# Performance work log

Hardware: AMD Instinct MI355X
Metric: run time of the kernel (lower is better)

The kernel has to match this reference:

```python
import jax, jax.numpy as jnp
import numpy as np

B, L, H = 4, 512, 768          # batch, seq_len, bert hidden
S, R = 100, 100                # num candidate spans, num relation pairs
E = 128                        # size embedding dim
TE, TR = 8, 6                  # entity / relation types
MAX_ENT_LEN = 100
NEG = -1e20


def _span_masks(rng, b, n, seq_len, max_len):
    # contiguous span masks with lengths in [1, max_len-1] so sum(-1) < max_len
    starts = rng.integers(0, seq_len - 1, size=(b, n))
    lengths = rng.integers(1, max_len, size=(b, n))
    ends = np.minimum(starts + lengths, seq_len)
    pos = np.arange(seq_len)
    m = (pos[None, None, :] >= starts[..., None]) & (pos[None, None, :] < ends[..., None])
    return jnp.asarray(m.astype(np.int32))


def setup_inputs() -> dict:
    rng = np.random.default_rng(0)
    key = jax.random.key(0)
    k = jax.random.split(key, 6)
    return {
        "last_hidden_state": jax.random.normal(k[0], (B, L, H), jnp.float32),
        "entity_mask": _span_masks(rng, B, S, L, MAX_ENT_LEN),
        "relations": jnp.asarray(rng.integers(0, S, size=(B, R, 2)).astype(np.int32)),
        "relation_context_mask": _span_masks(rng, B, R, L, MAX_ENT_LEN),
        "relation_sample_mask": jnp.asarray(rng.integers(0, 2, size=(B, R)).astype(np.int32)),
        "size_emb": jax.random.normal(k[1], (MAX_ENT_LEN, E), jnp.float32) * 0.02,
        "span_w": jax.random.normal(k[2], (E + 2 * H, TE), jnp.float32) * 0.02,
        "span_b": jnp.zeros((TE,), jnp.float32),
        "rel_w": jax.random.normal(k[3], (2 * E + 3 * H, TR), jnp.float32) * 0.02,
        "rel_b": jnp.zeros((TR,), jnp.float32),
    }


def _masked_max(h, mask):
    # h: [B,L,H], mask: [B,N,L] int {0,1} -> [B,N,H]
    mf = mask[..., None].astype(h.dtype)                       # [B,N,L,1]
    masked = jnp.where(mf == 0, jnp.asarray(NEG, h.dtype), h[:, None] * mf)
    return masked.max(axis=2)


def reference(last_hidden_state, entity_mask, relations, relation_context_mask,
              relation_sample_mask, size_emb, span_w, span_b, rel_w, rel_b):
    b = last_hidden_state.shape[0]
    # ---- entity classification ----
    context = last_hidden_state[:, 0]                          # CLS pooling [B,H]
    entity_size = size_emb[entity_mask.sum(-1)]                # [B,S,E]
    entity = _masked_max(last_hidden_state, entity_mask)       # [B,S,H]
    ctx = jnp.broadcast_to(context[:, None], (b, entity.shape[1], context.shape[-1]))
    entity_repr = jnp.concatenate([entity, ctx, entity_size], axis=-1)
    entity_logit = entity_repr @ span_w + span_b               # [B,S,TE]
    # ---- relation classification ----
    rel_ctx = _masked_max(last_hidden_state, relation_context_mask)  # [B,R,H]
    rel_ctx = jnp.where(relation_sample_mask[..., None] == 1,
                        jnp.zeros((), rel_ctx.dtype), rel_ctx)
    r = relations.shape[1]
    flat = relations.reshape(b, r * 2)                         # [B,2R]
    pair = jnp.take_along_axis(entity, flat[..., None], axis=1).reshape(b, r, -1)      # [B,R,2H]
    pair_size = jnp.take_along_axis(entity_size, flat[..., None], axis=1).reshape(b, r, -1)  # [B,R,2E]
    relation_repr = jnp.concatenate([rel_ctx, pair, pair_size], axis=-1)
    relation_logit = relation_repr @ rel_w + rel_b             # [B,R,TR]
    return entity_logit, relation_logit
```

## Files before the change

### kernel.cpp

```cpp
#include <hip/hip_runtime.h>

#define Bn 4
#define Ln 512
#define Hn 768
#define Sn 100
#define Rn 100
#define En 128
#define TEn 8
#define TRn 6
#define NEGF (-1e20f)
#define H4 (Hn / 4)
#define E4 (En / 4)
#define NTHR 640

__device__ __forceinline__ float4 fmax4(float4 a, float4 b) {
    return make_float4(fmaxf(a.x, b.x), fmaxf(a.y, b.y),
                       fmaxf(a.z, b.z), fmaxf(a.w, b.w));
}

__device__ __forceinline__ void scan_span(const int* __restrict__ mask,
                                          int lane, int* start, int* end) {
    const int4* m4 = (const int4*)(mask + lane * 8);
    int4 a = m4[0], c = m4[1];
    int mm[8] = {a.x, a.y, a.z, a.w, c.x, c.y, c.z, c.w};
    int first = 0x7fffffff, last = -1;
    #pragma unroll
    for (int r = 0; r < 8; ++r) {
        if (mm[r] != 0) {
            int row = lane * 8 + r;
            first = min(first, row);
            last = max(last, row);
        }
    }
    #pragma unroll
    for (int off = 1; off < 64; off <<= 1) {
        first = min(first, __shfl_xor(first, off, 64));
        last = max(last, __shfl_xor(last, off, 64));
    }
    *start = first;
    *end = last + 1;
}

__global__ void __launch_bounds__(NTHR)
span_kernel(const float* __restrict__ hid,
            const int* __restrict__ ent_mask,
            const int* __restrict__ rel_mask,
            const int* __restrict__ samp_mask,
            const float* __restrict__ size_emb,
            const float* __restrict__ span_w,
            const float* __restrict__ span_b,
            const float* __restrict__ rel_w,
            float* __restrict__ relpart,
            float* __restrict__ p0ws,
            float* __restrict__ p1ws,
            int* __restrict__ entcnt,
            float* __restrict__ out_ent) {
    int blk = blockIdx.x;
    int tid = threadIdx.x;
    int lane = tid & 63, wv = tid >> 6;
    int grp = tid / 192;
    int u = tid - grp * 192;

    __shared__ float4 sh[3][192];
    __shared__ float red[10][TEn];

    bool is_ent = blk < Bn * Sn;
    int b, rblk = 0;
    const int* mask;
    if (is_ent) {
        b = blk / Sn;
        mask = ent_mask + (size_t)blk * Ln;
    } else {
        rblk = blk - Bn * Sn;
        b = rblk / Rn;
        if (samp_mask[rblk] == 1) {
            if (tid < TRn) relpart[(size_t)rblk * TRn + tid] = 0.f;
            return;
        }
        mask = rel_mask + (size_t)rblk * Ln;
    }

    int start, end;
    scan_span(mask, lane, &start, &end);
    int cnt = end - start;
    if (is_ent && tid == 0) entcnt[blk] = cnt;

    const float4* hb4 = (const float4*)(hid + (size_t)b * Ln * Hn);

    if (grp < 3) {
        const float4* col = hb4 + u;
        float4 m0 = make_float4(NEGF, NEGF, NEGF, NEGF), m1 = m0;
        int r = start + grp;
        for (; r + 3 < end; r += 6) {
            m0 = fmax4(m0, col[(size_t)r * H4]);
            m1 = fmax4(m1, col[(size_t)(r + 3) * H4]);
        }
        if (r < end) m0 = fmax4(m0, col[(size_t)r * H4]);
        sh[grp][u] = fmax4(m0, m1);
    }
    __syncthreads();

    float acc[TEn];
    #pragma unroll
    for (int t = 0; t < TEn; ++t) acc[t] = 0.f;

    bool do_red;
    if (grp < 3) {
        do_red = is_ent || (grp == 0);
        if (do_red) {
            float4 v = fmax4(fmax4(sh[0][u], sh[1][u]), sh[2][u]);
            const float* vp = &v.x;
            if (is_ent) {
                if (grp == 0) {
                    #pragma unroll
                    for (int j = 0; j < 4; ++j) {
                        const float* wr = span_w + (size_t)(4 * u + j) * TEn;
                        #pragma unroll
                        for (int t = 0; t < TEn; ++t) acc[t] += vp[j] * wr[t];
                    }
                } else {
                    int base = (grp == 1 ? Hn : 2 * Hn) + 4 * u;
                    #pragma unroll
                    for (int j = 0; j < 4; ++j) {
                        const float* wr = rel_w + (size_t)(base + j) * TRn;
                        #pragma unroll
                        for (int t = 0; t < TRn; ++t) acc[t] += vp[j] * wr[t];
                    }
                }
            } else {
                #pragma unroll
                for (int j = 0; j < 4; ++j) {
                    const float* wr = rel_w + (size_t)(4 * u + j) * TRn;
                    #pragma unroll
                    for (int t = 0; t < TRn; ++t) acc[t] += vp[j] * wr[t];
                }
            }
        }
    } else {
        do_red = is_ent;
        if (is_ent) {
            #pragma unroll
            for (int cc = 0; cc < 3; ++cc) {
                int c = lane + cc * 64;
                float4 v = hb4[c];
                const float* vp = &v.x;
                #pragma unroll
                for (int j = 0; j < 4; ++j) {
                    const float* wr = span_w + (size_t)(Hn + 4 * c + j) * TEn;
                    #pragma unroll
                    for (int t = 0; t < TEn; ++t) acc[t] += vp[j] * wr[t];
                }
            }
            if (lane < E4) {
                float4 sv = ((const float4*)(size_emb + (size_t)cnt * En))[lane];
                const float* sp = &sv.x;
                #pragma unroll
                for (int j = 0; j < 4; ++j) {
                    const float* wr = span_w + (size_t)(2 * Hn + 4 * lane + j) * TEn;
                    #pragma unroll
                    for (int t = 0; t < TEn; ++t) acc[t] += sp[j] * wr[t];
                }
            }
        }
    }

    if (do_red) {
        #pragma unroll
        for (int t = 0; t < TEn; ++t)
            #pragma unroll
            for (int off = 32; off > 0; off >>= 1)
                acc[t] += __shfl_down(acc[t], off, 64);
        if (lane == 0) {
            #pragma unroll
            for (int t = 0; t < TEn; ++t) red[wv][t] = acc[t];
        }
    }
    __syncthreads();

    if (is_ent) {
        if (tid < TEn) {
            out_ent[(size_t)blk * TEn + tid] = span_b[tid]
                + red[0][tid] + red[1][tid] + red[2][tid] + red[9][tid];
        } else if (tid >= 64 && tid < 64 + TRn) {
            int t = tid - 64;
            p0ws[(size_t)blk * TRn + t] = red[3][t] + red[4][t] + red[5][t];
        } else if (tid >= 128 && tid < 128 + TRn) {
            int t = tid - 128;
            p1ws[(size_t)blk * TRn + t] = red[6][t] + red[7][t] + red[8][t];
        }
    } else {
        if (tid < TRn)
            relpart[(size_t)rblk * TRn + tid] =
                red[0][tid] + red[1][tid] + red[2][tid];
    }
}

__global__ void __launch_bounds__(64)
combine_kernel(const int* __restrict__ relations,
               const int* __restrict__ entcnt,
               const float* __restrict__ size_emb,
               const float* __restrict__ rel_w,
               const float* __restrict__ rel_b,
               const float* __restrict__ relpart,
               const float* __restrict__ p0ws,
               const float* __restrict__ p1ws,
               float* __restrict__ out_rel) {
    int rblk = blockIdx.x;
    int b = rblk / Rn;
    int lane = threadIdx.x;
    int a0 = relations[rblk * 2 + 0];
    int a1 = relations[rblk * 2 + 1];
    int e0 = b * Sn + a0, e1 = b * Sn + a1;

    int c = lane & 31;
    int srow = entcnt[(lane < 32) ? e0 : e1];
    int wbase = (lane < 32) ? 3 * Hn : 3 * Hn + En;

    float acc[TRn];
    #pragma unroll
    for (int t = 0; t < TRn; ++t) acc[t] = 0.f;

    float4 sv = ((const float4*)(size_emb + (size_t)srow * En))[c];
    const float* sp = &sv.x;
    #pragma unroll
    for (int j = 0; j < 4; ++j) {
        const float* wr = rel_w + (size_t)(wbase + 4 * c + j) * TRn;
        #pragma unroll
        for (int t = 0; t < TRn; ++t) acc[t] += sp[j] * wr[t];
    }

    #pragma unroll
    for (int t = 0; t < TRn; ++t)
        #pragma unroll
        for (int off = 32; off > 0; off >>= 1)
            acc[t] += __shfl_down(acc[t], off, 64);

    if (lane == 0) {
        #pragma unroll
        for (int t = 0; t < TRn; ++t) {
            out_rel[(size_t)rblk * TRn + t] = acc[t]
                + relpart[(size_t)rblk * TRn + t]
                + p0ws[(size_t)e0 * TRn + t]
                + p1ws[(size_t)e1 * TRn + t]
                + rel_b[t];
        }
    }
}

extern "C" void kernel_launch(void* const* d_in, const int* in_sizes, int n_in,
                              void* d_out, int out_size, void* d_ws, size_t ws_size,
                              hipStream_t stream) {
    const float* hid       = (const float*)d_in[0];
    const int*   ent_mask  = (const int*)d_in[1];
    const int*   relations = (const int*)d_in[2];
    const int*   rel_mask  = (const int*)d_in[3];
    const int*   samp_mask = (const int*)d_in[4];
    const float* size_emb  = (const float*)d_in[5];
    const float* span_w    = (const float*)d_in[6];
    const float* span_b    = (const float*)d_in[7];
    const float* rel_w     = (const float*)d_in[8];
    const float* rel_b     = (const float*)d_in[9];

    float* out = (float*)d_out;
    float* out_ent = out;
    float* out_rel = out + Bn * Sn * TEn;

    char* ws = (char*)d_ws;
    float* relpart = (float*)ws;
    float* p0ws    = relpart + (size_t)Bn * Rn * TRn;
    float* p1ws    = p0ws + (size_t)Bn * Sn * TRn;
    int*   entcnt  = (int*)(p1ws + (size_t)Bn * Sn * TRn);

    span_kernel<<<Bn * (Sn + Rn), NTHR, 0, stream>>>(
        hid, ent_mask, rel_mask, samp_mask, size_emb, span_w, span_b,
        rel_w, relpart, p0ws, p1ws, entcnt, out_ent);

    combine_kernel<<<Bn * Rn, 64, 0, stream>>>(
        relations, entcnt, size_emb, rel_w, rel_b,
        relpart, p0ws, p1ws, out_rel);
}
```

Baseline: 25.06 us.

## Precompute 8-row block maxima and fold pair-size projections into span kernel

Adds a pre-pass kernel that computes per-8-row block maxima of the hidden states, so each span's masked max reads block maxima for its interior and raw rows only at the ragged edges. The per-entity size-embedding projections onto the relation weights are moved into the span kernel's fourth-group waves. This lets the combine kernel become a simple elementwise gather-add over relations. It trades an extra launch plus a full pass over the hidden tensor for fewer per-span row reads and a lighter final kernel.

```diff
diff --git a/kernel.cpp b/kernel.cpp
--- a/kernel.cpp
+++ b/kernel.cpp
@@ -9,6 +9,8 @@
 #define TEn 8
 #define TRn 6
 #define NEGF (-1e20f)
+#define W 8
+#define NBLK (Ln / W)
 #define H4 (Hn / 4)
 #define E4 (En / 4)
 #define NTHR 640
@@ -16,6 +18,22 @@
 __device__ __forceinline__ float4 fmax4(float4 a, float4 b) {
     return make_float4(fmaxf(a.x, b.x), fmaxf(a.y, b.y),
                        fmaxf(a.z, b.z), fmaxf(a.w, b.w));
+}
+
+__global__ void __launch_bounds__(192)
+blockmax_kernel(const float* __restrict__ hid, float* __restrict__ bmax) {
+    int bj = blockIdx.x;
+    int b = bj / NBLK, j = bj % NBLK;
+    int tid = threadIdx.x;
+    const float4* src = (const float4*)(hid + ((size_t)b * Ln + j * W) * Hn);
+    float4 m0 = src[tid];
+    float4 m1 = src[(size_t)H4 + tid];
+    #pragma unroll
+    for (int r = 2; r < W; r += 2) {
+        m0 = fmax4(m0, src[(size_t)r * H4 + tid]);
+        m1 = fmax4(m1, src[(size_t)(r + 1) * H4 + tid]);
+    }
+    ((float4*)(bmax + (size_t)bj * Hn))[tid] = fmax4(m0, m1);
 }
 
 __device__ __forceinline__ void scan_span(const int* __restrict__ mask,
@@ -39,6 +57,28 @@
     }
     *start = first;
     *end = last + 1;
+}
+
+__device__ __forceinline__ float4 gmax(const float4* __restrict__ hb4,
+                                       const float4* __restrict__ bm4,
+                                       int start, int end, int grp) {
+    float4 m0 = make_float4(NEGF, NEGF, NEGF, NEGF), m1 = m0;
+    int jstart = (start + 7) >> 3, jend = end >> 3;
+    if (jstart >= jend) {
+        for (int r = start + grp; r < end; r += 6) {
+            m0 = fmax4(m0, hb4[(size_t)r * H4]);
+            int r2 = r + 3;
+            if (r2 < end) m1 = fmax4(m1, hb4[(size_t)r2 * H4]);
+        }
+        return fmax4(m0, m1);
+    }
+    for (int j = jstart + grp; j < jend; j += 3)
+        m0 = fmax4(m0, bm4[(size_t)j * H4]);
+    for (int r = start + grp; r < jstart * W; r += 3)
+        m1 = fmax4(m1, hb4[(size_t)r * H4]);
+    for (int r = jend * W + grp; r < end; r += 3)
+        m0 = fmax4(m0, hb4[(size_t)r * H4]);
+    return fmax4(m0, m1);
 }
 
 __global__ void __launch_bounds__(NTHR)
@@ -50,10 +90,10 @@
             const float* __restrict__ span_w,
             const float* __restrict__ span_b,
             const float* __restrict__ rel_w,
+            const float* __restrict__ bmax,
             float* __restrict__ relpart,
             float* __restrict__ p0ws,
             float* __restrict__ p1ws,
-            int* __restrict__ entcnt,
             float* __restrict__ out_ent) {
     int blk = blockIdx.x;
     int tid = threadIdx.x;
@@ -62,7 +102,8 @@
     int u = tid - grp * 192;
 
     __shared__ float4 sh[3][192];
-    __shared__ float red[10][TEn];
+    __shared__ float redA[9][TEn];
+    __shared__ float redW[3][TEn];
 
     bool is_ent = blk < Bn * Sn;
     int b, rblk = 0;
@@ -83,31 +124,24 @@
     int start, end;
     scan_span(mask, lane, &start, &end);
     int cnt = end - start;
-    if (is_ent && tid == 0) entcnt[blk] = cnt;
 
     const float4* hb4 = (const float4*)(hid + (size_t)b * Ln * Hn);
+    const float4* bm4 = (const float4*)(bmax + (size_t)b * NBLK * Hn);
+
+    if (grp < 3)
+        sh[grp][u] = gmax(hb4 + u, bm4 + u, start, end, grp);
+    __syncthreads();
+
+    float acc[TEn];
+    #pragma unroll
+    for (int t = 0; t < TEn; ++t) acc[t] = 0.f;
+    float acc2[TRn], acc3[TRn];
+    #pragma unroll
+    for (int t = 0; t < TRn; ++t) { acc2[t] = 0.f; acc3[t] = 0.f; }
 
     if (grp < 3) {
-        const float4* col = hb4 + u;
-        float4 m0 = make_float4(NEGF, NEGF, NEGF, NEGF), m1 = m0;
-        int r = start + grp;
-        for (; r + 3 < end; r += 6) {
-            m0 = fmax4(m0, col[(size_t)r * H4]);
-            m1 = fmax4(m1, col[(size_t)(r + 3) * H4]);
-        }
-        if (r < end) m0 = fmax4(m0, col[(size_t)r * H4]);
-        sh[grp][u] = fmax4(m0, m1);
-    }
-    __syncthreads();
-
-    float acc[TEn];
-    #pragma unroll
-    for (int t = 0; t < TEn; ++t) acc[t] = 0.f;
-
-    bool do_red;
-    if (grp < 3) {
-        do_red = is_ent || (grp == 0);
-        if (do_red) {
+        bool active = is_ent || (grp == 0);
+        if (active) {
             float4 v = fmax4(fmax4(sh[0][u], sh[1][u]), sh[2][u]);
             const float* vp = &v.x;
             if (is_ent) {
@@ -136,35 +170,6 @@
                 }
             }
         }
-    } else {
-        do_red = is_ent;
-        if (is_ent) {
-            #pragma unroll
-            for (int cc = 0; cc < 3; ++cc) {
-                int c = lane + cc * 64;
-                float4 v = hb4[c];
-                const float* vp = &v.x;
-                #pragma unroll
-                for (int j = 0; j < 4; ++j) {
-                    const float* wr = span_w + (size_t)(Hn + 4 * c + j) * TEn;
-                    #pragma unroll
-                    for (int t = 0; t < TEn; ++t) acc[t] += vp[j] * wr[t];
-                }
-            }
-            if (lane < E4) {
-                float4 sv = ((const float4*)(size_emb + (size_t)cnt * En))[lane];
-                const float* sp = &sv.x;
-                #pragma unroll
-                for (int j = 0; j < 4; ++j) {
-                    const float* wr = span_w + (size_t)(2 * Hn + 4 * lane + j) * TEn;
-                    #pragma unroll
-                    for (int t = 0; t < TEn; ++t) acc[t] += sp[j] * wr[t];
-                }
-            }
-        }
-    }
-
-    if (do_red) {
         #pragma unroll
         for (int t = 0; t < TEn; ++t)
             #pragma unroll
@@ -172,7 +177,54 @@
                 acc[t] += __shfl_down(acc[t], off, 64);
         if (lane == 0) {
             #pragma unroll
-            for (int t = 0; t < TEn; ++t) red[wv][t] = acc[t];
+            for (int t = 0; t < TEn; ++t) redA[wv][t] = acc[t];
+        }
+    } else if (is_ent) {
+        #pragma unroll
+        for (int cc = 0; cc < 3; ++cc) {
+            int c = lane + cc * 64;
+            float4 v = hb4[c];
+            const float* vp = &v.x;
+            #pragma unroll
+            for (int j = 0; j < 4; ++j) {
+                const float* wr = span_w + (size_t)(Hn + 4 * c + j) * TEn;
+                #pragma unroll
+                for (int t = 0; t < TEn; ++t) acc[t] += vp[j] * wr[t];
+            }
+        }
+        if (lane < E4) {
+            float4 sv = ((const float4*)(size_emb + (size_t)cnt * En))[lane];
+            const float* sp = &sv.x;
+            #pragma unroll
+            for (int j = 0; j < 4; ++j) {
+                const float* w1 = span_w + (size_t)(2 * Hn + 4 * lane + j) * TEn;
+                const float* w2 = rel_w + (size_t)(3 * Hn + 4 * lane + j) * TRn;
+                const float* w3 = rel_w + (size_t)(3 * Hn + En + 4 * lane + j) * TRn;
+                #pragma unroll
+                for (int t = 0; t < TEn; ++t) acc[t] += sp[j] * w1[t];
+                #pragma unroll
+                for (int t = 0; t < TRn; ++t) { acc2[t] += sp[j] * w2[t];
+                                                acc3[t] += sp[j] * w3[t]; }
+            }
+        }
+        #pragma unroll
+        for (int t = 0; t < TEn; ++t)
+            #pragma unroll
+            for (int off = 32; off > 0; off >>= 1)
+                acc[t] += __shfl_down(acc[t], off, 64);
+        #pragma unroll
+        for (int t = 0; t < TRn; ++t)
+            #pragma unroll
+            for (int off = 32; off > 0; off >>= 1) {
+                acc2[t] += __shfl_down(acc2[t], off, 64);
+                acc3[t] += __shfl_down(acc3[t], off, 64);
+            }
+        if (lane == 0) {
+            #pragma unroll
+            for (int t = 0; t < TEn; ++t) redW[0][t] = acc[t];
+            #pragma unroll
+            for (int t = 0; t < TRn; ++t) { redW[1][t] = acc2[t];
+                                            redW[2][t] = acc3[t]; }
         }
     }
     __syncthreads();
@@ -180,71 +232,40 @@
     if (is_ent) {
         if (tid < TEn) {
             out_ent[(size_t)blk * TEn + tid] = span_b[tid]
-                + red[0][tid] + red[1][tid] + red[2][tid] + red[9][tid];
+                + redA[0][tid] + redA[1][tid] + redA[2][tid] + redW[0][tid];
         } else if (tid >= 64 && tid < 64 + TRn) {
             int t = tid - 64;
-            p0ws[(size_t)blk * TRn + t] = red[3][t] + red[4][t] + red[5][t];
+            p0ws[(size_t)blk * TRn + t] =
+                redA[3][t] + redA[4][t] + redA[5][t] + redW[1][t];
         } else if (tid >= 128 && tid < 128 + TRn) {
             int t = tid - 128;
-            p1ws[(size_t)blk * TRn + t] = red[6][t] + red[7][t] + red[8][t];
+            p1ws[(size_t)blk * TRn + t] =
+                redA[6][t] + redA[7][t] + redA[8][t] + redW[2][t];
         }
     } else {
         if (tid < TRn)
             relpart[(size_t)rblk * TRn + tid] =
-                red[0][tid] + red[1][tid] + red[2][tid];
-    }
-}
-
-__global__ void __launch_bounds__(64)
+                redA[0][tid] + redA[1][tid] + redA[2][tid];
+    }
+}
+
+__global__ void __launch_bounds__(256)
 combine_kernel(const int* __restrict__ relations,
-               const int* __restrict__ entcnt,
-               const float* __restrict__ size_emb,
-               const float* __restrict__ rel_w,
                const float* __restrict__ rel_b,
                const float* __restrict__ relpart,
                const float* __restrict__ p0ws,
                const float* __restrict__ p1ws,
                float* __restrict__ out_rel) {
-    int rblk = blockIdx.x;
-    int b = rblk / Rn;
-    int lane = threadIdx.x;
-    int a0 = relations[rblk * 2 + 0];
-    int a1 = relations[rblk * 2 + 1];
-    int e0 = b * Sn + a0, e1 = b * Sn + a1;
-
-    int c = lane & 31;
-    int srow = entcnt[(lane < 32) ? e0 : e1];
-    int wbase = (lane < 32) ? 3 * Hn : 3 * Hn + En;
-
-    float acc[TRn];
-    #pragma unroll
-    for (int t = 0; t < TRn; ++t) acc[t] = 0.f;
-
-    float4 sv = ((const float4*)(size_emb + (size_t)srow * En))[c];
-    const float* sp = &sv.x;
-    #pragma unroll
-    for (int j = 0; j < 4; ++j) {
-        const float* wr = rel_w + (size_t)(wbase + 4 * c + j) * TRn;
-        #pragma unroll
-        for (int t = 0; t < TRn; ++t) acc[t] += sp[j] * wr[t];
-    }
-
-    #pragma unroll
-    for (int t = 0; t < TRn; ++t)
-        #pragma unroll
-        for (int off = 32; off > 0; off >>= 1)
-            acc[t] += __shfl_down(acc[t], off, 64);
-
-    if (lane == 0) {
-        #pragma unroll
-        for (int t = 0; t < TRn; ++t) {
-            out_rel[(size_t)rblk * TRn + t] = acc[t]
-                + relpart[(size_t)rblk * TRn + t]
-                + p0ws[(size_t)e0 * TRn + t]
-                + p1ws[(size_t)e1 * TRn + t]
-                + rel_b[t];
-        }
-    }
+    int idx = blockIdx.x * 256 + threadIdx.x;
+    if (idx >= Bn * Rn * TRn) return;
+    int r = idx / TRn, t = idx - r * TRn;
+    int b = r / Rn;
+    int a0 = relations[r * 2 + 0];
+    int a1 = relations[r * 2 + 1];
+    out_rel[idx] = relpart[idx]
+        + p0ws[(size_t)(b * Sn + a0) * TRn + t]
+        + p1ws[(size_t)(b * Sn + a1) * TRn + t]
+        + rel_b[t];
 }
 
 extern "C" void kernel_launch(void* const* d_in, const int* in_sizes, int n_in,
@@ -266,16 +287,17 @@
     float* out_rel = out + Bn * Sn * TEn;
 
     char* ws = (char*)d_ws;
-    float* relpart = (float*)ws;
+    float* bmax    = (float*)ws;
+    float* relpart = bmax + (size_t)Bn * NBLK * Hn;
     float* p0ws    = relpart + (size_t)Bn * Rn * TRn;
     float* p1ws    = p0ws + (size_t)Bn * Sn * TRn;
-    int*   entcnt  = (int*)(p1ws + (size_t)Bn * Sn * TRn);
+
+    blockmax_kernel<<<Bn * NBLK, 192, 0, stream>>>(hid, bmax);
 
     span_kernel<<<Bn * (Sn + Rn), NTHR, 0, stream>>>(
         hid, ent_mask, rel_mask, samp_mask, size_emb, span_w, span_b,
-        rel_w, relpart, p0ws, p1ws, entcnt, out_ent);
-
-    combine_kernel<<<Bn * Rn, 64, 0, stream>>>(
-        relations, entcnt, size_emb, rel_w, rel_b,
-        relpart, p0ws, p1ws, out_rel);
-}
+        rel_w, bmax, relpart, p0ws, p1ws, out_ent);
+
+    combine_kernel<<<(Bn * Rn * TRn + 255) / 256, 256, 0, stream>>>(
+        relations, rel_b, relpart, p0ws, p1ws, out_rel);
+}
```

Measured after the change: 23.81 us. -5.0%, faster.
